# Optimization experiments

Measured on AMD Instinct MI355X. Metric: run time of the kernel, lower is better.

Reference implementation:

```python
import jax, jax.numpy as jnp
import numpy as np

NUM_HEADS = 64
NUM_HEADS_KV = 1
HEAD_SIZE = 64
HIDDEN = NUM_HEADS * HEAD_SIZE  # 4096
SOFTMAX_SCALE = HEAD_SIZE ** -0.5
BATCH = 4
SEQ = 1024
TOTAL = BATCH * SEQ


def setup_inputs() -> dict:
    key = jax.random.key(0)
    k1, k2, k3, k4, k5 = jax.random.split(key, 5)
    hidden_states = jax.random.normal(k1, (TOTAL, HIDDEN), dtype=jnp.float32)
    # rotary cos/sin per token position (head_size/2 features, rotate-half style)
    pos = jnp.tile(jnp.arange(SEQ, dtype=jnp.float32), BATCH)  # [TOTAL]
    inv_freq = 1.0 / (10000.0 ** (jnp.arange(0, HEAD_SIZE, 2, dtype=jnp.float32) / HEAD_SIZE))
    freqs = pos[:, None] * inv_freq[None, :]  # [TOTAL, 32]
    cos = jnp.cos(freqs)
    sin = jnp.sin(freqs)
    w_qkv = jax.random.normal(k2, (HIDDEN, HIDDEN + 2 * NUM_HEADS_KV * HEAD_SIZE), dtype=jnp.float32) * (HIDDEN ** -0.5)
    w_dense = jax.random.normal(k3, (HIDDEN, HIDDEN), dtype=jnp.float32) * (HIDDEN ** -0.5)
    cu_seqlen_prefill = jnp.arange(BATCH + 1, dtype=jnp.int32) * SEQ
    return {
        "hidden_states": hidden_states,
        "cos": cos,
        "sin": sin,
        "w_qkv": w_qkv,
        "w_dense": w_dense,
        "cu_seqlen_prefill": cu_seqlen_prefill,
    }


def _rope(x, cos, sin):
    # x: [T, H, D]; cos/sin: [T, D/2]; rotate-half pairing (x1=first half, x2=second half)
    d2 = x.shape[-1] // 2
    x1, x2 = x[..., :d2], x[..., d2:]
    c = cos[:, None, :]
    s = sin[:, None, :]
    return jnp.concatenate([x1 * c - x2 * s, x2 * c + x1 * s], axis=-1)


def reference(hidden_states, cos, sin, w_qkv, w_dense, cu_seqlen_prefill):
    T = hidden_states.shape[0]
    B = cu_seqlen_prefill.shape[0] - 1
    S = T // B
    qkv = hidden_states @ w_qkv  # [T, H*D + 2*D]
    q = qkv[:, : NUM_HEADS * HEAD_SIZE].reshape(T, NUM_HEADS, HEAD_SIZE)
    kv = qkv[:, NUM_HEADS * HEAD_SIZE:].reshape(T, 2, NUM_HEADS_KV, HEAD_SIZE)
    k = kv[:, 0]  # [T, 1, D]
    v = kv[:, 1]
    q = _rope(q, cos, sin)
    k = _rope(k, cos, sin)
    # ragged sequences of equal length -> batch view (prefill flash-attn path, causal)
    qb = q.reshape(B, S, NUM_HEADS, HEAD_SIZE)
    kb = k.reshape(B, S, NUM_HEADS_KV, HEAD_SIZE)[:, :, 0]  # MQA: single kv head [B,S,D]
    vb = v.reshape(B, S, NUM_HEADS_KV, HEAD_SIZE)[:, :, 0]
    scores = jnp.einsum("bshd,btd->bhst", qb, kb) * SOFTMAX_SCALE  # [B,H,S,S]
    causal = jnp.tril(jnp.ones((S, S), dtype=bool))
    scores = jnp.where(causal[None, None], scores, jnp.finfo(scores.dtype).min)
    p = jax.nn.softmax(scores, axis=-1)
    out = jnp.einsum("bhst,btd->bshd", p, vb)  # [B,S,H,D]
    out = out.reshape(T, NUM_HEADS * HEAD_SIZE)
    return out @ w_dense
```

## Files before the change

kernel.cpp:

```cpp
#include <hip/hip_runtime.h>
#include <hip/hip_bf16.h>
#include <stdint.h>

#define HID   4096
#define NQKV  4224
#define TOT   4096
#define SEQq  1024
#define NH    64
#define HD    64
#define SM_SCALE 0.125f
#define LOG2E 1.44269504088896f

typedef float  f32x4  __attribute__((ext_vector_type(4)));
typedef short  short8 __attribute__((ext_vector_type(8)));
typedef ushort ushort4v __attribute__((ext_vector_type(4)));

static __device__ __forceinline__ ushort f2bf(float f) {
    uint32_t u = __float_as_uint(f);
    u += 0x7FFFu + ((u >> 16) & 1u);
    return (ushort)(u >> 16);
}

static __device__ __forceinline__ void gload_lds16(const void* g, void* l) {
    __builtin_amdgcn_global_load_lds(
        (const __attribute__((address_space(1))) uint32_t*)g,
        (__attribute__((address_space(3))) uint32_t*)l, 16, 0, 0);
}

__global__ __launch_bounds__(256) void cast_bf16_kernel(
    const float* __restrict__ in, ushort* __restrict__ out, int n4)
{
    int i = blockIdx.x * 256 + threadIdx.x;
    if (i < n4) {
        float4 v = ((const float4*)in)[i];
        ushort4v o;
        o.x = f2bf(v.x); o.y = f2bf(v.y); o.z = f2bf(v.z); o.w = f2bf(v.w);
        ((ushort4v*)out)[i] = o;
    }
}

__global__ __launch_bounds__(256) void transpose_cast_kernel(
    const float* __restrict__ in, ushort* __restrict__ out, int R, int C)
{
    __shared__ float tile[32][33];
    int c0 = blockIdx.x * 32, r0 = blockIdx.y * 32;
    int tx = threadIdx.x & 31, ty = threadIdx.x >> 5;
#pragma unroll
    for (int i = 0; i < 4; i++)
        tile[ty + i * 8][tx] = in[(size_t)(r0 + ty + i * 8) * C + c0 + tx];
    __syncthreads();
#pragma unroll
    for (int i = 0; i < 4; i++)
        out[(size_t)(c0 + ty + i * 8) * R + r0 + tx] = f2bf(tile[tx][ty + i * 8]);
}

#define BUFSZ 49152
template<int EPI>
__global__ __launch_bounds__(512, 1) void gemm2_kernel(
    const ushort* __restrict__ A, const ushort* __restrict__ B,
    float* __restrict__ Cf, ushort* __restrict__ qkv, ushort* __restrict__ vt,
    const float* __restrict__ cosT, const float* __restrict__ sinT,
    int M, int N, int K, int MB)
{
    extern __shared__ char lds[];
    const int tid = threadIdx.x;
    const int lane = tid & 63, wave = tid >> 6;
    const int wm = wave >> 1, wn = wave & 1;

    const int nwg = gridDim.x;
    const int cpx = nwg >> 3;
    const int id2 = (blockIdx.x & 7) * cpx + (blockIdx.x >> 3);
    const int by = id2 % MB, bx = id2 / MB;
    const int m0 = by * 256, n0 = bx * 128;

    f32x4 acc[4][4] = {};

    const int srow = tid >> 3;
    const int scw  = ((tid & 7) ^ (srow & 7)) << 3;
    const ushort* Abase = A + (size_t)m0 * K;
    const ushort* Bbase = B + (size_t)n0 * K;
    const int NT = K >> 6;

#define STAGE(t)  {                                                          \
        char* buf = lds + ((t) % 3) * BUFSZ;                                 \
        const int k0 = (t) << 6;                                             \
        _Pragma("unroll")                                                    \
        for (int a = 0; a < 4; a++)                                          \
            gload_lds16(Abase + (size_t)(a * 64 + srow) * K + k0 + scw,      \
                        buf + a * 8192 + wave * 1024);                       \
        _Pragma("unroll")                                                    \
        for (int b2 = 0; b2 < 2; b2++)                                       \
            gload_lds16(Bbase + (size_t)(b2 * 64 + srow) * K + k0 + scw,     \
                        buf + 32768 + b2 * 8192 + wave * 1024);              \
    }

    STAGE(0);
    STAGE(1);

    for (int t = 0; t < NT; t++) {
        if (t + 1 < NT)
            asm volatile("s_waitcnt vmcnt(6)" ::: "memory");
        else
            asm volatile("s_waitcnt vmcnt(0)" ::: "memory");
        __builtin_amdgcn_s_barrier();
        asm volatile("" ::: "memory");
        if (t + 2 < NT) STAGE(t + 2);

        const char* bufA = lds + (t % 3) * BUFSZ;
        const char* bufB = bufA + 32768;
        short8 af[4][2], bfr[4][2];
#pragma unroll
        for (int ks = 0; ks < 2; ks++) {
            const int cb = (ks * 64 + ((lane >> 4) << 4)) ^ ((lane & 7) << 4);
#pragma unroll
            for (int m = 0; m < 4; m++)
                af[m][ks] = *(const short8*)(bufA +
                    (wm * 64 + m * 16 + (lane & 15)) * 128 + cb);
#pragma unroll
            for (int n = 0; n < 4; n++)
                bfr[n][ks] = *(const short8*)(bufB +
                    (wn * 64 + n * 16 + (lane & 15)) * 128 + cb);
        }
        __builtin_amdgcn_s_setprio(1);
#pragma unroll
        for (int ks = 0; ks < 2; ks++)
#pragma unroll
            for (int m = 0; m < 4; m++)
#pragma unroll
                for (int n = 0; n < 4; n++)
                    acc[m][n] = __builtin_amdgcn_mfma_f32_16x16x32_bf16(
                        af[m][ks], bfr[n][ks], acc[m][n], 0, 0, 0);
        __builtin_amdgcn_s_setprio(0);
    }
#undef STAGE

    if (EPI == 0) {
#pragma unroll
        for (int m = 0; m < 4; m++) {
            int row = m0 + wm * 64 + m * 16 + ((lane >> 4) << 2);
#pragma unroll
            for (int n = 0; n < 4; n++) {
                int col = n0 + wn * 64 + n * 16 + (lane & 15);
#pragma unroll
                for (int j = 0; j < 4; j++)
                    Cf[(size_t)(row + j) * N + col] = acc[m][n][j];
            }
        }
    } else {
        const int cn = n0 + wn * 64;
        if (cn < HID + HD) {
#pragma unroll
            for (int m = 0; m < 4; m++)
#pragma unroll
                for (int j = 0; j < 4; j++) {
                    int t = m0 + wm * 64 + m * 16 + ((lane >> 4) << 2) + j;
#pragma unroll
                    for (int n = 0; n < 2; n++) {
                        int d = n * 16 + (lane & 15);
                        float c = cosT[t * 32 + d];
                        float s = sinT[t * 32 + d];
                        float x1 = acc[m][n][j], x2 = acc[m][n + 2][j];
                        qkv[(size_t)t * NQKV + cn + d]      = f2bf(x1 * c - x2 * s);
                        qkv[(size_t)t * NQKV + cn + d + 32] = f2bf(x2 * c + x1 * s);
                    }
                }
        } else {
#pragma unroll
            for (int m = 0; m < 4; m++)
#pragma unroll
                for (int n = 0; n < 4; n++)
#pragma unroll
                    for (int j = 0; j < 4; j++) {
                        int t = m0 + wm * 64 + m * 16 + ((lane >> 4) << 2) + j;
                        int d = n * 16 + (lane & 15);
                        vt[(size_t)((t >> 10) * 64 + d) * SEQq + (t & 1023)] =
                            f2bf(acc[m][n][j]);
                    }
        }
    }
}

__global__ __launch_bounds__(256) void attn_kernel(
    const ushort* __restrict__ qkv, const ushort* __restrict__ vt,
    ushort* __restrict__ aout)
{
    __shared__ char plds[16384];
    const int lane = threadIdx.x & 63, wave = threadIdx.x >> 6;
    const int qb = blockIdx.x, h = blockIdx.y, b = blockIdx.z;
    const int q0 = qb * 128 + wave * 32;
    char* pbase = plds + wave * 4096;

    short8 aq[2][2];
#pragma unroll
    for (int m = 0; m < 2; m++)
#pragma unroll
        for (int ks = 0; ks < 2; ks++)
            aq[m][ks] = *(const short8*)(qkv +
                (size_t)(b * SEQq + q0 + m * 16 + (lane & 15)) * NQKV +
                h * HD + ks * 32 + ((lane >> 4) << 3));

    f32x4 o[2][4] = {};
    float Lp[2][4] = {};
    const float Cs = SM_SCALE * LOG2E;

    const int kvend = q0 + 32;
    for (int kv0 = 0; kv0 < kvend; kv0 += 64) {
        f32x4 sc[2][4] = {};
#pragma unroll
        for (int ks = 0; ks < 2; ks++) {
            short8 bk[4];
#pragma unroll
            for (int n = 0; n < 4; n++)
                bk[n] = *(const short8*)(qkv +
                    (size_t)(b * SEQq + kv0 + n * 16 + (lane & 15)) * NQKV +
                    HID + ks * 32 + ((lane >> 4) << 3));
#pragma unroll
            for (int m = 0; m < 2; m++)
#pragma unroll
                for (int n = 0; n < 4; n++)
                    sc[m][n] = __builtin_amdgcn_mfma_f32_16x16x32_bf16(
                        aq[m][ks], bk[n], sc[m][n], 0, 0, 0);
        }
#pragma unroll
        for (int m = 0; m < 2; m++)
#pragma unroll
            for (int n = 0; n < 4; n++) {
                int kvg = kv0 + n * 16 + (lane & 15);
#pragma unroll
                for (int j = 0; j < 4; j++) {
                    int qg = q0 + m * 16 + ((lane >> 4) << 2) + j;
                    float e = __builtin_amdgcn_exp2f(sc[m][n][j] * Cs);
                    float p = (kvg <= qg) ? e : 0.f;
                    Lp[m][j] += p;
                    int qq = m * 16 + ((lane >> 4) << 2) + j;
                    *(ushort*)(pbase + qq * 128 +
                        (((n * 16 + (lane & 15)) * 2) ^ ((qq & 7) << 4))) = f2bf(p);
                }
            }
#pragma unroll
        for (int ks2 = 0; ks2 < 2; ks2++) {
            short8 pa[2], vb[4];
#pragma unroll
            for (int m = 0; m < 2; m++)
                pa[m] = *(const short8*)(pbase + (m * 16 + (lane & 15)) * 128 +
                    ((ks2 * 64 + ((lane >> 4) << 4)) ^ ((lane & 7) << 4)));
#pragma unroll
            for (int n = 0; n < 4; n++)
                vb[n] = *(const short8*)(vt +
                    (size_t)(b * 64 + n * 16 + (lane & 15)) * SEQq +
                    kv0 + ks2 * 32 + ((lane >> 4) << 3));
#pragma unroll
            for (int m = 0; m < 2; m++)
#pragma unroll
                for (int n = 0; n < 4; n++)
                    o[m][n] = __builtin_amdgcn_mfma_f32_16x16x32_bf16(
                        pa[m], vb[n], o[m][n], 0, 0, 0);
        }
    }

#pragma unroll
    for (int m = 0; m < 2; m++)
#pragma unroll
        for (int j = 0; j < 4; j++) {
            float L = Lp[m][j];
            L += __shfl_xor(L, 1);
            L += __shfl_xor(L, 2);
            L += __shfl_xor(L, 4);
            L += __shfl_xor(L, 8);
            float inv = 1.f / L;
            int t = b * SEQq + q0 + m * 16 + ((lane >> 4) << 2) + j;
#pragma unroll
            for (int n = 0; n < 4; n++)
                aout[(size_t)t * HID + h * HD + n * 16 + (lane & 15)] =
                    f2bf(o[m][n][j] * inv);
        }
}

extern "C" void kernel_launch(void* const* d_in, const int* in_sizes, int n_in,
                              void* d_out, int out_size, void* d_ws, size_t ws_size,
                              hipStream_t stream)
{
    const float* hidden  = (const float*)d_in[0];
    const float* cosT    = (const float*)d_in[1];
    const float* sinT    = (const float*)d_in[2];
    const float* w_qkv   = (const float*)d_in[3];
    const float* w_dense = (const float*)d_in[4];
    float* out = (float*)d_out;

    char* ws = (char*)d_ws;
    ushort* hB   = (ushort*)(ws);
    ushort* wqT  = (ushort*)(ws + 33554432);
    ushort* wdT  = (ushort*)(ws + 68157440);
    ushort* qkvB = (ushort*)(ws + 101711872);
    ushort* vtB  = (ushort*)(ws + 136314880);
    ushort* aoB  = (ushort*)(ws + 136839168);

    hipFuncSetAttribute((const void*)gemm2_kernel<1>,
                        hipFuncAttributeMaxDynamicSharedMemorySize, 3 * BUFSZ);
    hipFuncSetAttribute((const void*)gemm2_kernel<0>,
                        hipFuncAttributeMaxDynamicSharedMemorySize, 3 * BUFSZ);

    cast_bf16_kernel<<<16384, 256, 0, stream>>>(hidden, hB, TOT * HID / 4);
    transpose_cast_kernel<<<dim3(NQKV / 32, HID / 32), 256, 0, stream>>>(
        w_qkv, wqT, HID, NQKV);
    transpose_cast_kernel<<<dim3(HID / 32, HID / 32), 256, 0, stream>>>(
        w_dense, wdT, HID, HID);
    gemm2_kernel<1><<<528, 512, 3 * BUFSZ, stream>>>(
        hB, wqT, nullptr, qkvB, vtB, cosT, sinT, TOT, NQKV, HID, TOT / 256);
    attn_kernel<<<dim3(8, NH, 4), 256, 0, stream>>>(qkvB, vtB, aoB);
    gemm2_kernel<0><<<512, 512, 3 * BUFSZ, stream>>>(
        aoB, wdT, out, nullptr, nullptr, nullptr, nullptr, TOT, HID, HID, TOT / 256);
}
```

Measured before the change: 779.8 us.

## Rebalance causal attention by pairing query tiles and transposing score layout

```diff
diff --git a/kernel.cpp b/kernel.cpp
--- a/kernel.cpp
+++ b/kernel.cpp
@@ -14,11 +14,18 @@
 typedef float  f32x4  __attribute__((ext_vector_type(4)));
 typedef short  short8 __attribute__((ext_vector_type(8)));
 typedef ushort ushort4v __attribute__((ext_vector_type(4)));
+typedef uint32_t uint2v __attribute__((ext_vector_type(2)));
 
 static __device__ __forceinline__ ushort f2bf(float f) {
     uint32_t u = __float_as_uint(f);
     u += 0x7FFFu + ((u >> 16) & 1u);
     return (ushort)(u >> 16);
+}
+
+static __device__ __forceinline__ uint32_t cvt_pk_bf16(float lo, float hi) {
+    uint32_t r;
+    asm("v_cvt_pk_bf16_f32 %0, %1, %2" : "=v"(r) : "v"(lo), "v"(hi));
+    return r;
 }
 
 static __device__ __forceinline__ void gload_lds16(const void* g, void* l) {
@@ -180,100 +187,119 @@
     }
 }
 
-__global__ __launch_bounds__(256) void attn_kernel(
+__global__ __launch_bounds__(256, 4) void attn_kernel(
     const ushort* __restrict__ qkv, const ushort* __restrict__ vt,
     ushort* __restrict__ aout)
 {
     __shared__ char plds[16384];
     const int lane = threadIdx.x & 63, wave = threadIdx.x >> 6;
-    const int qb = blockIdx.x, h = blockIdx.y, b = blockIdx.z;
-    const int q0 = qb * 128 + wave * 32;
+    const int h = blockIdx.y, b = blockIdx.z;
     char* pbase = plds + wave * 4096;
-
-    short8 aq[2][2];
-#pragma unroll
-    for (int m = 0; m < 2; m++)
-#pragma unroll
-        for (int ks = 0; ks < 2; ks++)
-            aq[m][ks] = *(const short8*)(qkv +
-                (size_t)(b * SEQq + q0 + m * 16 + (lane & 15)) * NQKV +
-                h * HD + ks * 32 + ((lane >> 4) << 3));
-
-    f32x4 o[2][4] = {};
-    float Lp[2][4] = {};
+    const int l15 = lane & 15, lg = lane >> 4;
     const float Cs = SM_SCALE * LOG2E;
 
-    const int kvend = q0 + 32;
-    for (int kv0 = 0; kv0 < kvend; kv0 += 64) {
-        f32x4 sc[2][4] = {};
-#pragma unroll
-        for (int ks = 0; ks < 2; ks++) {
-            short8 bk[4];
-#pragma unroll
-            for (int n = 0; n < 4; n++)
-                bk[n] = *(const short8*)(qkv +
-                    (size_t)(b * SEQq + kv0 + n * 16 + (lane & 15)) * NQKV +
-                    HID + ks * 32 + ((lane >> 4) << 3));
-#pragma unroll
-            for (int m = 0; m < 2; m++)
-#pragma unroll
-                for (int n = 0; n < 4; n++)
-                    sc[m][n] = __builtin_amdgcn_mfma_f32_16x16x32_bf16(
-                        aq[m][ks], bk[n], sc[m][n], 0, 0, 0);
-        }
-#pragma unroll
-        for (int m = 0; m < 2; m++)
-#pragma unroll
-            for (int n = 0; n < 4; n++) {
-                int kvg = kv0 + n * 16 + (lane & 15);
-#pragma unroll
-                for (int j = 0; j < 4; j++) {
-                    int qg = q0 + m * 16 + ((lane >> 4) << 2) + j;
-                    float e = __builtin_amdgcn_exp2f(sc[m][n][j] * Cs);
-                    float p = (kvg <= qg) ? e : 0.f;
-                    Lp[m][j] += p;
-                    int qq = m * 16 + ((lane >> 4) << 2) + j;
-                    *(ushort*)(pbase + qq * 128 +
-                        (((n * 16 + (lane & 15)) * 2) ^ ((qq & 7) << 4))) = f2bf(p);
+    for (int pass = 0; pass < 2; pass++) {
+        const int qt = (pass == 0) ? blockIdx.x : 7 - blockIdx.x;
+        const int q0 = qt * 128 + wave * 32;
+
+        short8 aq[2][2];
+#pragma unroll
+        for (int n = 0; n < 2; n++)
+#pragma unroll
+            for (int ks = 0; ks < 2; ks++)
+                aq[n][ks] = *(const short8*)(qkv +
+                    (size_t)(b * SEQq + q0 + n * 16 + l15) * NQKV +
+                    h * HD + ks * 32 + lg * 8);
+
+        f32x4 oT[4][2] = {};
+        float Lp[2] = {};
+        const int nfull = q0 >> 6;
+
+        for (int t = 0; t <= nfull; t++) {
+            const int kv0 = t << 6;
+            const bool diag = (t == nfull);
+            const int mh = diag ? ((q0 & 32) ? 4 : 2) : 4;
+
+            f32x4 scT[4][2] = {};
+#pragma unroll
+            for (int ks = 0; ks < 2; ks++) {
+                short8 bk[4];
+                for (int m = 0; m < mh; m++)
+                    bk[m] = *(const short8*)(qkv +
+                        (size_t)(b * SEQq + kv0 + m * 16 + l15) * NQKV +
+                        HID + ks * 32 + lg * 8);
+                for (int m = 0; m < mh; m++)
+#pragma unroll
+                    for (int n = 0; n < 2; n++)
+                        scT[m][n] = __builtin_amdgcn_mfma_f32_16x16x32_bf16(
+                            bk[m], aq[n][ks], scT[m][n], 0, 0, 0);
+            }
+
+            for (int m = 0; m < mh; m++)
+#pragma unroll
+                for (int n = 0; n < 2; n++) {
+                    float p4[4];
+#pragma unroll
+                    for (int j = 0; j < 4; j++) {
+                        float e = __builtin_amdgcn_exp2f(scT[m][n][j] * Cs);
+                        if (diag) {
+                            int kvg = kv0 + m * 16 + lg * 4 + j;
+                            int qg  = q0 + n * 16 + l15;
+                            e = (kvg <= qg) ? e : 0.f;
+                        }
+                        Lp[n] += e;
+                        p4[j] = e;
+                    }
+                    uint2v pk;
+                    pk.x = cvt_pk_bf16(p4[0], p4[1]);
+                    pk.y = cvt_pk_bf16(p4[2], p4[3]);
+                    int q = n * 16 + l15;
+                    int kb = m * 32 + lg * 8;
+                    *(uint2v*)(pbase + q * 128 +
+                               ((((kb >> 4) ^ (q & 7)) << 4) | (kb & 15))) = pk;
                 }
+
+            for (int ks2 = 0; ks2 < (mh >> 1); ks2++) {
+                short8 vb[4], pb[2];
+#pragma unroll
+                for (int md = 0; md < 4; md++)
+                    vb[md] = *(const short8*)(vt +
+                        (size_t)(b * 64 + md * 16 + l15) * SEQq +
+                        kv0 + ks2 * 32 + lg * 8);
+#pragma unroll
+                for (int no = 0; no < 2; no++) {
+                    int q = no * 16 + l15;
+                    pb[no] = *(const short8*)(pbase + q * 128 +
+                        (((ks2 * 4 + lg) ^ (q & 7)) << 4));
+                }
+#pragma unroll
+                for (int md = 0; md < 4; md++)
+#pragma unroll
+                    for (int no = 0; no < 2; no++)
+                        oT[md][no] = __builtin_amdgcn_mfma_f32_16x16x32_bf16(
+                            vb[md], pb[no], oT[md][no], 0, 0, 0);
             }
-#pragma unroll
-        for (int ks2 = 0; ks2 < 2; ks2++) {
-            short8 pa[2], vb[4];
-#pragma unroll
-            for (int m = 0; m < 2; m++)
-                pa[m] = *(const short8*)(pbase + (m * 16 + (lane & 15)) * 128 +
-                    ((ks2 * 64 + ((lane >> 4) << 4)) ^ ((lane & 7) << 4)));
-#pragma unroll
-            for (int n = 0; n < 4; n++)
-                vb[n] = *(const short8*)(vt +
-                    (size_t)(b * 64 + n * 16 + (lane & 15)) * SEQq +
-                    kv0 + ks2 * 32 + ((lane >> 4) << 3));
-#pragma unroll
-            for (int m = 0; m < 2; m++)
-#pragma unroll
-                for (int n = 0; n < 4; n++)
-                    o[m][n] = __builtin_amdgcn_mfma_f32_16x16x32_bf16(
-                        pa[m], vb[n], o[m][n], 0, 0, 0);
-        }
-    }
-
-#pragma unroll
-    for (int m = 0; m < 2; m++)
-#pragma unroll
-        for (int j = 0; j < 4; j++) {
-            float L = Lp[m][j];
-            L += __shfl_xor(L, 1);
-            L += __shfl_xor(L, 2);
-            L += __shfl_xor(L, 4);
-            L += __shfl_xor(L, 8);
-            float inv = 1.f / L;
-            int t = b * SEQq + q0 + m * 16 + ((lane >> 4) << 2) + j;
-#pragma unroll
-            for (int n = 0; n < 4; n++)
-                aout[(size_t)t * HID + h * HD + n * 16 + (lane & 15)] =
-                    f2bf(o[m][n][j] * inv);
-        }
+        }
+
+        float inv[2];
+#pragma unroll
+        for (int no = 0; no < 2; no++) {
+            float L = Lp[no];
+            L += __shfl_xor(L, 16);
+            L += __shfl_xor(L, 32);
+            inv[no] = 1.f / L;
+        }
+#pragma unroll
+        for (int md = 0; md < 4; md++)
+#pragma unroll
+            for (int no = 0; no < 2; no++) {
+                uint2v s;
+                s.x = cvt_pk_bf16(oT[md][no][0] * inv[no], oT[md][no][1] * inv[no]);
+                s.y = cvt_pk_bf16(oT[md][no][2] * inv[no], oT[md][no][3] * inv[no]);
+                int tq = b * SEQq + q0 + no * 16 + l15;
+                *(uint2v*)(aout + (size_t)tq * HID + h * HD + md * 16 + lg * 4) = s;
+            }
+    }
 }
 
 extern "C" void kernel_launch(void* const* d_in, const int* in_sizes, int n_in,
@@ -307,7 +333,7 @@
         w_dense, wdT, HID, HID);
     gemm2_kernel<1><<<528, 512, 3 * BUFSZ, stream>>>(
         hB, wqT, nullptr, qkvB, vtB, cosT, sinT, TOT, NQKV, HID, TOT / 256);
-    attn_kernel<<<dim3(8, NH, 4), 256, 0, stream>>>(qkvB, vtB, aoB);
+    attn_kernel<<<dim3(4, NH, 4), 256, 0, stream>>>(qkvB, vtB, aoB);
     gemm2_kernel<0><<<512, 512, 3 * BUFSZ, stream>>>(
         aoB, wdT, out, nullptr, nullptr, nullptr, nullptr, TOT, HID, HID, TOT / 256);
 }
```

Measured after the change: 764.1 us. 1.02x faster.
